# Performance work log

Hardware: AMD Instinct MI355X
Metric: run time of the kernel (lower is better)

## Reference

```python
import jax, jax.numpy as jnp
import numpy as np


def setup_inputs() -> dict:
    key = jax.random.key(0)
    k1, k2 = jax.random.split(key)
    n_nodes, d_feat, n_edges = 100000, 48, 1600000
    x = jax.random.normal(k1, (n_nodes, d_feat), dtype=jnp.float32)
    edge_index = jax.random.randint(k2, (2, n_edges), 0, n_nodes, dtype=jnp.int64)
    return {"x": x, "edge_index": edge_index, "batch_size": 65536}


def reference(x, edge_index, batch_size):
    # adj = SparseTensor.from_edge_index(edge_index): adj[row, col] = 1 with
    # row = edge_index[0] (src), col = edge_index[1] (dst).
    # adj.t() @ x  ->  out[i] = sum over edges (src -> i) of x[src]
    src, dst = edge_index[0], edge_index[1]
    n_nodes = x.shape[0]
    # memory-bound gather + scatter-add (SpMM, sum aggregation)
    x_neighbors_sum = jax.ops.segment_sum(x[src], dst, num_segments=n_nodes)
    node_labels = jnp.concatenate(
        (x[:batch_size, :], x_neighbors_sum[:batch_size, :]), axis=-1
    )
    return node_labels
```

## Files before the change

kernel.cpp:

```cpp
#include <hip/hip_runtime.h>
#include <hip/hip_fp16.h>

#define DFEAT 48
#define OUTW  96
#define NBINB 512
#define BINTH 512
#define EPT   7
#define SORTCAP 3584
#define NBUCK2 512
#define RBITS 7
#define NROWS 128
#define RAWCAP 2560
#define CSRCAP 2560


static __device__ __forceinline__ unsigned short f2h(float f) {
    __half h = __float2half_rn(f);
    return *reinterpret_cast<unsigned short*>(&h);
}

static __device__ __forceinline__ int wave_iscan(int v, int lane) {
    #pragma unroll
    for (int d = 1; d < 64; d <<= 1) {
        int tv = __shfl_up(v, d, 64);
        if (lane >= d) v += tv;
    }
    return v;
}

__global__ __launch_bounds__(BINTH)
void bin_k(const int* __restrict__ ei, int n_edges, int batch, int chunk,
           const float4* __restrict__ x4, int nx4, uint2* __restrict__ xh4,
           unsigned short* __restrict__ starts, unsigned int* __restrict__ regions,
           float4* __restrict__ out4, int use_half) {
    __shared__ int cnt[NBUCK2];
    __shared__ int cur[NBUCK2];
    __shared__ int wsum[BINTH / 64];
    __shared__ int totS;
    __shared__ unsigned int sorted[SORTCAP];
    const int t = threadIdx.x;
    const int b = blockIdx.x;
    const int lane = t & 63, wid = t >> 6;

    if (use_half) {
        const int batch12 = batch * 12;
        for (int i = b * BINTH + t; i < nx4; i += NBINB * BINTH) {
            float4 v = x4[i];
            xh4[i] = make_uint2((unsigned)f2h(v.x) | ((unsigned)f2h(v.y) << 16),
                                (unsigned)f2h(v.z) | ((unsigned)f2h(v.w) << 16));
            if (i < batch12) {
                int row = i / 12, cg = i - row * 12;
                out4[(size_t)row * 24 + cg] = v;
            }
        }
    }

    const int beg = b * chunk;
    const int end = min(beg + chunk, n_edges);

    unsigned int pay[EPT];
    int bkt[EPT];
    #pragma unroll
    for (int i = 0; i < EPT; i++) {
        bkt[i] = -1;
        int e = beg + t + i * BINTH;
        if (e < end) {
            int dst = ei[n_edges + e];
            if (dst < batch) {
                int src = ei[e];
                bkt[i] = dst >> RBITS;
                pay[i] = ((unsigned)(dst & (NROWS - 1)) << 17) | (unsigned)src;
            }
        }
    }
    cnt[t] = 0;
    __syncthreads();
    #pragma unroll
    for (int i = 0; i < EPT; i++)
        if (bkt[i] >= 0) atomicAdd(&cnt[bkt[i]], 1);
    __syncthreads();
    int v = cnt[t];
    int iv = wave_iscan(v, lane);
    if (lane == 63) wsum[wid] = iv;
    __syncthreads();
    if (t < BINTH / 64) {
        int wv = wsum[t];
        int sv = wave_iscan(wv, t);
        wsum[t] = sv - wv;
        if (t == BINTH / 64 - 1) totS = sv;
    }
    __syncthreads();
    int excl = iv - v + wsum[wid];
    int tot = totS;
    cur[t] = excl;
    starts[t * NBINB + b] = (unsigned short)excl;
    if (t == 0) starts[NBUCK2 * NBINB + b] = (unsigned short)tot;
    __syncthreads();
    #pragma unroll
    for (int i = 0; i < EPT; i++)
        if (bkt[i] >= 0) {
            int pos = atomicAdd(&cur[bkt[i]], 1);
            sorted[pos] = pay[i];
        }
    __syncthreads();
    unsigned int* reg = regions + (size_t)b * chunk;
    for (int i = t; i < tot; i += BINTH) reg[i] = sorted[i];
}

__global__ __launch_bounds__(1024)
void reduce_k(const float* __restrict__ x, const uint2* __restrict__ xh2,
              const unsigned short* __restrict__ starts,
              const unsigned int* __restrict__ regions,
              float* __restrict__ out, int batch, int chunk, int use_half) {
    __shared__ unsigned int raw[RAWCAP];
    __shared__ int csr[CSRCAP];
    __shared__ int cnt[NROWS], off[NROWS + 1], cur[NROWS];
    __shared__ int rbase[NBINB], rs[NBINB], rl[NBINB];
    __shared__ int wsum[16];
    __shared__ int totS;
    const int t = threadIdx.x;
    const int kb = blockIdx.x;
    const int lane = t & 63, wid = t >> 6;

    int s0 = 0, len = 0;
    if (t < NBINB) {
        s0 = starts[kb * NBINB + t];
        int s1 = starts[(kb + 1) * NBINB + t];
        len = s1 - s0;
    }
    int iv = wave_iscan(len, lane);
    if (lane == 63 && wid < 8) wsum[wid] = iv;
    __syncthreads();
    if (t < 8) {
        int wv = wsum[t];
        int sv = wave_iscan(wv, t);
        wsum[t] = sv - wv;
        if (t == 7) totS = sv;
    }
    __syncthreads();
    if (t < NBINB) {
        rbase[t] = iv - len + wsum[wid];
        rs[t] = s0;
        rl[t] = len;
    }
    __syncthreads();
    const int T = min(totS, RAWCAP);
    {
        int r = t >> 1, h = t & 1;
        int L = rl[r], base = rbase[r];
        const unsigned int* reg = regions + (size_t)r * chunk + rs[r];
        if (L <= 8) {
            #pragma unroll
            for (int i = 0; i < 4; i++) {
                int idx = h + 2 * i;
                if (idx < L) {
                    int p = base + idx;
                    if (p < RAWCAP) raw[p] = reg[idx];
                }
            }
        } else {
            for (int idx = h; idx < L; idx += 2) {
                int p = base + idx;
                if (p < RAWCAP) raw[p] = reg[idx];
            }
        }
    }
    if (t < NROWS) cnt[t] = 0;
    __syncthreads();
    for (int i = t; i < T; i += 1024) atomicAdd(&cnt[raw[i] >> 17], 1);
    __syncthreads();
    int v2 = (t < NROWS) ? cnt[t] : 0;
    int iv2 = wave_iscan(v2, lane);
    if (lane == 63 && wid < 2) wsum[wid] = iv2;
    __syncthreads();
    if (t == 0) {
        int a = wsum[0];
        off[NROWS] = a + wsum[1];
        wsum[1] = a;
        wsum[0] = 0;
    }
    __syncthreads();
    if (t < NROWS) {
        int excl = iv2 - v2 + wsum[wid];
        off[t] = excl;
        cur[t] = excl;
    }
    __syncthreads();
    for (int i = t; i < T; i += 1024) {
        unsigned int p = raw[i];
        int pos = atomicAdd(&cur[p >> 17], 1);
        if (pos < CSRCAP) csr[pos] = (int)(p & 0x1FFFFu) * 12;
    }
    __syncthreads();

    if (use_half) {
        const int g  = lane / 12;
        const int cg = lane - g * 12;
        const bool act = lane < 48;
        float4* out4 = (float4*)out;
        #pragma unroll
        for (int rr = 0; rr < 4; rr++) {
            const int ra = wid + 16 * rr;
            const int rb = ra + 64;
            const int rowA = kb * NROWS + ra;
            const int rowB = kb * NROWS + rb;
            const bool okA = rowA < batch, okB = rowB < batch;
            int e0a = 0, e1a = 0, e0b = 0, e1b = 0;
            if (okA) { e0a = off[ra]; e1a = min(off[ra + 1], CSRCAP); }
            if (okB) { e0b = off[rb]; e1b = min(off[rb + 1], CSRCAP); }
            float4 accA = make_float4(0.f, 0.f, 0.f, 0.f);
            float4 accB = make_float4(0.f, 0.f, 0.f, 0.f);
            int na = e1a - e0a, nb2 = e1b - e0b;
            int n = na > nb2 ? na : nb2;
            for (int k = 0; k < n; k += 8) {
                if (act) {
                    int a1 = e0a + k + g, a2 = e0a + k + 4 + g;
                    int b1 = e0b + k + g, b2 = e0b + k + 4 + g;
                    if (a1 < e1a) {
                        uint2 p = xh2[(size_t)csr[a1] + cg];
                        float2 f0 = __half22float2(*(const __half2*)&p.x);
                        float2 f1 = __half22float2(*(const __half2*)&p.y);
                        accA.x += f0.x; accA.y += f0.y; accA.z += f1.x; accA.w += f1.y;
                    }
                    if (b1 < e1b) {
                        uint2 p = xh2[(size_t)csr[b1] + cg];
                        float2 f0 = __half22float2(*(const __half2*)&p.x);
                        float2 f1 = __half22float2(*(const __half2*)&p.y);
                        accB.x += f0.x; accB.y += f0.y; accB.z += f1.x; accB.w += f1.y;
                    }
                    if (a2 < e1a) {
                        uint2 p = xh2[(size_t)csr[a2] + cg];
                        float2 f0 = __half22float2(*(const __half2*)&p.x);
                        float2 f1 = __half22float2(*(const __half2*)&p.y);
                        accA.x += f0.x; accA.y += f0.y; accA.z += f1.x; accA.w += f1.y;
                    }
                    if (b2 < e1b) {
                        uint2 p = xh2[(size_t)csr[b2] + cg];
                        float2 f0 = __half22float2(*(const __half2*)&p.x);
                        float2 f1 = __half22float2(*(const __half2*)&p.y);
                        accB.x += f0.x; accB.y += f0.y; accB.z += f1.x; accB.w += f1.y;
                    }
                }
            }
            float4 bb;
            bb.x = __shfl(accA.x, lane + 24); bb.y = __shfl(accA.y, lane + 24);
            bb.z = __shfl(accA.z, lane + 24); bb.w = __shfl(accA.w, lane + 24);
            if (lane < 24) { accA.x += bb.x; accA.y += bb.y; accA.z += bb.z; accA.w += bb.w; }
            bb.x = __shfl(accA.x, lane + 12); bb.y = __shfl(accA.y, lane + 12);
            bb.z = __shfl(accA.z, lane + 12); bb.w = __shfl(accA.w, lane + 12);
            if (lane < 12 && okA) {
                accA.x += bb.x; accA.y += bb.y; accA.z += bb.z; accA.w += bb.w;
                out4[(size_t)rowA * 24 + 12 + cg] = accA;
            }
            bb.x = __shfl(accB.x, lane + 24); bb.y = __shfl(accB.y, lane + 24);
            bb.z = __shfl(accB.z, lane + 24); bb.w = __shfl(accB.w, lane + 24);
            if (lane < 24) { accB.x += bb.x; accB.y += bb.y; accB.z += bb.z; accB.w += bb.w; }
            bb.x = __shfl(accB.x, lane + 12); bb.y = __shfl(accB.y, lane + 12);
            bb.z = __shfl(accB.z, lane + 12); bb.w = __shfl(accB.w, lane + 12);
            if (lane < 12 && okB) {
                accB.x += bb.x; accB.y += bb.y; accB.z += bb.z; accB.w += bb.w;
                out4[(size_t)rowB * 24 + 12 + cg] = accB;
            }
        }
    } else {
        if (lane < DFEAT) {
            for (int r = wid; r < NROWS; r += 16) {
                int row = kb * NROWS + r;
                if (row >= batch) break;
                int e0 = off[r], e1 = min(off[r + 1], CSRCAP);
                float acc = 0.f;
                for (int e = e0; e < e1; ++e)
                    acc += x[(size_t)csr[e] * 4 + lane];
                out[(size_t)row * OUTW + lane]         = x[(size_t)row * DFEAT + lane];
                out[(size_t)row * OUTW + DFEAT + lane] = acc;
            }
        }
    }
}


#define D4   12
#define ROW4 24

__global__ void init_out_kernel(const float4* __restrict__ x4,
                                float4* __restrict__ out4, int batch) {
    int idx = blockIdx.x * blockDim.x + threadIdx.x;
    int total = batch * ROW4;
    if (idx >= total) return;
    int row = idx / ROW4;
    int c   = idx - row * ROW4;
    float4 v;
    if (c < D4) v = x4[row * D4 + c];
    else        v = make_float4(0.f, 0.f, 0.f, 0.f);
    out4[idx] = v;
}

__global__ void scatter_edges_kernel(const float4* __restrict__ x4,
                                     const int* __restrict__ ei,
                                     float* __restrict__ out,
                                     int n_edges, int batch) {
    int tid = blockIdx.x * blockDim.x + threadIdx.x;
    int e = tid / D4;
    int q = tid - e * D4;
    if (e >= n_edges) return;
    int dst = ei[n_edges + e];
    if (dst >= batch) return;
    int src = ei[e];
    float4 v = x4[src * D4 + q];
    float* p = out + (size_t)dst * OUTW + DFEAT + q * 4;
    atomicAdd(p + 0, v.x);
    atomicAdd(p + 1, v.y);
    atomicAdd(p + 2, v.z);
    atomicAdd(p + 3, v.w);
}


extern "C" void kernel_launch(void* const* d_in, const int* in_sizes, int n_in,
                              void* d_out, int out_size, void* d_ws, size_t ws_size,
                              hipStream_t stream) {
    const float* x  = (const float*)d_in[0];
    const int*   ei = (const int*)d_in[1];
    float* out = (float*)d_out;

    const int n_edges = in_sizes[1] / 2;
    const int batch   = out_size / OUTW;
    const int n_nodes = in_sizes[0] / DFEAT;
    const int chunk   = (n_edges + NBINB - 1) / NBINB;
    const int nbuck   = (batch + NROWS - 1) / NROWS;
    const int nx4     = n_nodes * DFEAT / 4;

    size_t xh_bytes = ((size_t)n_nodes * DFEAT * sizeof(unsigned short) + 15) & ~(size_t)15;
    size_t starts_bytes = (size_t)(NBUCK2 + 1) * NBINB * sizeof(unsigned short);
    size_t reg_bytes = (size_t)NBINB * chunk * sizeof(unsigned int);
    size_t need_h = xh_bytes + starts_bytes + reg_bytes;
    size_t need_f = starts_bytes + reg_bytes;

    bool base_ok = chunk <= SORTCAP && chunk <= BINTH * EPT && chunk < 65536 &&
                   n_nodes <= (1 << 17) && batch <= NBUCK2 * NROWS &&
                   (n_nodes * DFEAT) % 4 == 0 && nbuck >= 1 && nbuck <= NBUCK2 &&
                   batch % NROWS == 0;

    if (base_ok && ws_size >= need_h) {
        unsigned short* xh = (unsigned short*)d_ws;
        unsigned short* starts = (unsigned short*)((char*)d_ws + xh_bytes);
        unsigned int* regions = (unsigned int*)((char*)d_ws + xh_bytes + starts_bytes);
        bin_k<<<NBINB, BINTH, 0, stream>>>(ei, n_edges, batch, chunk,
                                           (const float4*)x, nx4, (uint2*)xh,
                                           starts, regions, (float4*)out, 1);
        reduce_k<<<nbuck, 1024, 0, stream>>>(x, (const uint2*)xh, starts, regions,
                                             out, batch, chunk, 1);
    } else if (base_ok && ws_size >= need_f) {
        unsigned short* starts = (unsigned short*)d_ws;
        unsigned int* regions = (unsigned int*)((char*)d_ws + starts_bytes);
        bin_k<<<NBINB, BINTH, 0, stream>>>(ei, n_edges, batch, chunk,
                                           (const float4*)x, nx4, (uint2*)0,
                                           starts, regions, (float4*)out, 0);
        reduce_k<<<nbuck, 1024, 0, stream>>>(x, (const uint2*)0, starts, regions,
                                             out, batch, chunk, 0);
    } else {
        {
            int total = batch * ROW4;
            int grid = (total + 255) / 256;
            init_out_kernel<<<grid, 256, 0, stream>>>((const float4*)x,
                                                      (float4*)out, batch);
        }
        {
            long long total = (long long)n_edges * D4;
            long long grid = (total + 255) / 256;
            scatter_edges_kernel<<<(int)grid, 256, 0, stream>>>(
                (const float4*)x, ei, out, n_edges, batch);
        }
    }
}
```

Baseline: 119.6 us.

## Fuse bin and reduce kernels via cooperative launch with grid sync

Merges the binning and per-row reduction kernels into one cooperative kernel that separates the phases with a grid-wide barrier, falling back to two launches when cooperative launch is unavailable or occupancy is insufficient. The reduce phase is templated on thread count so it can run with 512 threads per block inside the fused kernel. The half-precision gather is also widened to 16-byte loads, with each edge split between A and B rows across half-waves. This removes one kernel launch and its boundary, at the cost of running the reduce phase with fewer threads per block and adding a grid barrier. The fp32 fallback's csr index scaling was also changed (stride 8 with a *6 row index), which looks inconsistent with that path.

```diff
diff --git a/kernel.cpp b/kernel.cpp
--- a/kernel.cpp
+++ b/kernel.cpp
@@ -1,5 +1,6 @@
 #include <hip/hip_runtime.h>
 #include <hip/hip_fp16.h>
+#include <hip/hip_cooperative_groups.h>
 
 #define DFEAT 48
 #define OUTW  96
@@ -28,18 +29,18 @@
     return v;
 }
 
-__global__ __launch_bounds__(BINTH)
-void bin_k(const int* __restrict__ ei, int n_edges, int batch, int chunk,
-           const float4* __restrict__ x4, int nx4, uint2* __restrict__ xh4,
-           unsigned short* __restrict__ starts, unsigned int* __restrict__ regions,
-           float4* __restrict__ out4, int use_half) {
+static __device__ __forceinline__ void bin_body(
+    const int* __restrict__ ei, int n_edges, int batch, int chunk,
+    const float4* __restrict__ x4, int nx4, uint2* __restrict__ xh4,
+    unsigned short* __restrict__ starts, unsigned int* __restrict__ regions,
+    float4* __restrict__ out4, int use_half, int b)
+{
     __shared__ int cnt[NBUCK2];
     __shared__ int cur[NBUCK2];
     __shared__ int wsum[BINTH / 64];
     __shared__ int totS;
     __shared__ unsigned int sorted[SORTCAP];
     const int t = threadIdx.x;
-    const int b = blockIdx.x;
     const int lane = t & 63, wid = t >> 6;
 
     if (use_half) {
@@ -107,11 +108,15 @@
     for (int i = t; i < tot; i += BINTH) reg[i] = sorted[i];
 }
 
-__global__ __launch_bounds__(1024)
-void reduce_k(const float* __restrict__ x, const uint2* __restrict__ xh2,
-              const unsigned short* __restrict__ starts,
-              const unsigned int* __restrict__ regions,
-              float* __restrict__ out, int batch, int chunk, int use_half) {
+template<int NT>
+static __device__ __forceinline__ void reduce_body(
+    const float* __restrict__ x, const uint4* __restrict__ xh4,
+    const unsigned short* __restrict__ starts,
+    const unsigned int* __restrict__ regions,
+    float* __restrict__ out, int batch, int chunk, int use_half, int kb)
+{
+    constexpr int NW  = NT / 64;
+    constexpr int TPR = NT / NBINB;
     __shared__ unsigned int raw[RAWCAP];
     __shared__ int csr[CSRCAP];
     __shared__ int cnt[NROWS], off[NROWS + 1], cur[NROWS];
@@ -119,7 +124,6 @@
     __shared__ int wsum[16];
     __shared__ int totS;
     const int t = threadIdx.x;
-    const int kb = blockIdx.x;
     const int lane = t & 63, wid = t >> 6;
 
     int s0 = 0, len = 0;
@@ -146,20 +150,11 @@
     __syncthreads();
     const int T = min(totS, RAWCAP);
     {
-        int r = t >> 1, h = t & 1;
-        int L = rl[r], base = rbase[r];
-        const unsigned int* reg = regions + (size_t)r * chunk + rs[r];
-        if (L <= 8) {
-            #pragma unroll
-            for (int i = 0; i < 4; i++) {
-                int idx = h + 2 * i;
-                if (idx < L) {
-                    int p = base + idx;
-                    if (p < RAWCAP) raw[p] = reg[idx];
-                }
-            }
-        } else {
-            for (int idx = h; idx < L; idx += 2) {
+        int r = t / TPR, h = t - r * TPR;
+        if (r < NBINB) {
+            int L = rl[r], base = rbase[r];
+            const unsigned int* reg = regions + (size_t)r * chunk + rs[r];
+            for (int idx = h; idx < L; idx += TPR) {
                 int p = base + idx;
                 if (p < RAWCAP) raw[p] = reg[idx];
             }
@@ -167,7 +162,7 @@
     }
     if (t < NROWS) cnt[t] = 0;
     __syncthreads();
-    for (int i = t; i < T; i += 1024) atomicAdd(&cnt[raw[i] >> 17], 1);
+    for (int i = t; i < T; i += NT) atomicAdd(&cnt[raw[i] >> 17], 1);
     __syncthreads();
     int v2 = (t < NROWS) ? cnt[t] : 0;
     int iv2 = wave_iscan(v2, lane);
@@ -186,21 +181,22 @@
         cur[t] = excl;
     }
     __syncthreads();
-    for (int i = t; i < T; i += 1024) {
+    for (int i = t; i < T; i += NT) {
         unsigned int p = raw[i];
         int pos = atomicAdd(&cur[p >> 17], 1);
-        if (pos < CSRCAP) csr[pos] = (int)(p & 0x1FFFFu) * 12;
+        if (pos < CSRCAP) csr[pos] = (int)(p & 0x1FFFFu) * 6;
     }
     __syncthreads();
 
     if (use_half) {
-        const int g  = lane / 12;
-        const int cg = lane - g * 12;
+        const int g   = lane / 6;
+        const int cg  = lane - g * 6;
         const bool act = lane < 48;
+        const bool isA = g < 4;
+        const int gg  = isA ? g : g - 4;
         float4* out4 = (float4*)out;
-        #pragma unroll
-        for (int rr = 0; rr < 4; rr++) {
-            const int ra = wid + 16 * rr;
+        for (int rr = 0; rr < 64 / NW; rr++) {
+            const int ra = wid + NW * rr;
             const int rb = ra + 64;
             const int rowA = kb * NROWS + ra;
             const int rowB = kb * NROWS + rb;
@@ -208,74 +204,99 @@
             int e0a = 0, e1a = 0, e0b = 0, e1b = 0;
             if (okA) { e0a = off[ra]; e1a = min(off[ra + 1], CSRCAP); }
             if (okB) { e0b = off[rb]; e1b = min(off[rb + 1], CSRCAP); }
-            float4 accA = make_float4(0.f, 0.f, 0.f, 0.f);
-            float4 accB = make_float4(0.f, 0.f, 0.f, 0.f);
-            int na = e1a - e0a, nb2 = e1b - e0b;
-            int n = na > nb2 ? na : nb2;
+            const int e0 = isA ? e0a : e0b;
+            const int e1 = isA ? e1a : e1b;
+            float a0=0.f,a1=0.f,a2=0.f,a3=0.f,a4=0.f,a5=0.f,a6=0.f,a7=0.f;
+            const int n = max(e1a - e0a, e1b - e0b);
             for (int k = 0; k < n; k += 8) {
-                if (act) {
-                    int a1 = e0a + k + g, a2 = e0a + k + 4 + g;
-                    int b1 = e0b + k + g, b2 = e0b + k + 4 + g;
-                    if (a1 < e1a) {
-                        uint2 p = xh2[(size_t)csr[a1] + cg];
-                        float2 f0 = __half22float2(*(const __half2*)&p.x);
-                        float2 f1 = __half22float2(*(const __half2*)&p.y);
-                        accA.x += f0.x; accA.y += f0.y; accA.z += f1.x; accA.w += f1.y;
-                    }
-                    if (b1 < e1b) {
-                        uint2 p = xh2[(size_t)csr[b1] + cg];
-                        float2 f0 = __half22float2(*(const __half2*)&p.x);
-                        float2 f1 = __half22float2(*(const __half2*)&p.y);
-                        accB.x += f0.x; accB.y += f0.y; accB.z += f1.x; accB.w += f1.y;
-                    }
-                    if (a2 < e1a) {
-                        uint2 p = xh2[(size_t)csr[a2] + cg];
-                        float2 f0 = __half22float2(*(const __half2*)&p.x);
-                        float2 f1 = __half22float2(*(const __half2*)&p.y);
-                        accA.x += f0.x; accA.y += f0.y; accA.z += f1.x; accA.w += f1.y;
-                    }
-                    if (b2 < e1b) {
-                        uint2 p = xh2[(size_t)csr[b2] + cg];
-                        float2 f0 = __half22float2(*(const __half2*)&p.x);
-                        float2 f1 = __half22float2(*(const __half2*)&p.y);
-                        accB.x += f0.x; accB.y += f0.y; accB.z += f1.x; accB.w += f1.y;
-                    }
+                int i1 = e0 + k + gg;
+                int i2 = i1 + 4;
+                if (act && i1 < e1) {
+                    uint4 p = xh4[(size_t)csr[i1] + cg];
+                    float2 f0 = __half22float2(*(const __half2*)&p.x);
+                    float2 f1 = __half22float2(*(const __half2*)&p.y);
+                    float2 f2 = __half22float2(*(const __half2*)&p.z);
+                    float2 f3 = __half22float2(*(const __half2*)&p.w);
+                    a0 += f0.x; a1 += f0.y; a2 += f1.x; a3 += f1.y;
+                    a4 += f2.x; a5 += f2.y; a6 += f3.x; a7 += f3.y;
                 }
-            }
-            float4 bb;
-            bb.x = __shfl(accA.x, lane + 24); bb.y = __shfl(accA.y, lane + 24);
-            bb.z = __shfl(accA.z, lane + 24); bb.w = __shfl(accA.w, lane + 24);
-            if (lane < 24) { accA.x += bb.x; accA.y += bb.y; accA.z += bb.z; accA.w += bb.w; }
-            bb.x = __shfl(accA.x, lane + 12); bb.y = __shfl(accA.y, lane + 12);
-            bb.z = __shfl(accA.z, lane + 12); bb.w = __shfl(accA.w, lane + 12);
-            if (lane < 12 && okA) {
-                accA.x += bb.x; accA.y += bb.y; accA.z += bb.z; accA.w += bb.w;
-                out4[(size_t)rowA * 24 + 12 + cg] = accA;
-            }
-            bb.x = __shfl(accB.x, lane + 24); bb.y = __shfl(accB.y, lane + 24);
-            bb.z = __shfl(accB.z, lane + 24); bb.w = __shfl(accB.w, lane + 24);
-            if (lane < 24) { accB.x += bb.x; accB.y += bb.y; accB.z += bb.z; accB.w += bb.w; }
-            bb.x = __shfl(accB.x, lane + 12); bb.y = __shfl(accB.y, lane + 12);
-            bb.z = __shfl(accB.z, lane + 12); bb.w = __shfl(accB.w, lane + 12);
-            if (lane < 12 && okB) {
-                accB.x += bb.x; accB.y += bb.y; accB.z += bb.z; accB.w += bb.w;
-                out4[(size_t)rowB * 24 + 12 + cg] = accB;
+                if (act && i2 < e1) {
+                    uint4 p = xh4[(size_t)csr[i2] + cg];
+                    float2 f0 = __half22float2(*(const __half2*)&p.x);
+                    float2 f1 = __half22float2(*(const __half2*)&p.y);
+                    float2 f2 = __half22float2(*(const __half2*)&p.z);
+                    float2 f3 = __half22float2(*(const __half2*)&p.w);
+                    a0 += f0.x; a1 += f0.y; a2 += f1.x; a3 += f1.y;
+                    a4 += f2.x; a5 += f2.y; a6 += f3.x; a7 += f3.y;
+                }
+            }
+            float b0,b1,b2,b3,b4,b5,b6,b7;
+            b0=__shfl(a0,lane+12); b1=__shfl(a1,lane+12);
+            b2=__shfl(a2,lane+12); b3=__shfl(a3,lane+12);
+            b4=__shfl(a4,lane+12); b5=__shfl(a5,lane+12);
+            b6=__shfl(a6,lane+12); b7=__shfl(a7,lane+12);
+            a0+=b0; a1+=b1; a2+=b2; a3+=b3; a4+=b4; a5+=b5; a6+=b6; a7+=b7;
+            b0=__shfl(a0,lane+6); b1=__shfl(a1,lane+6);
+            b2=__shfl(a2,lane+6); b3=__shfl(a3,lane+6);
+            b4=__shfl(a4,lane+6); b5=__shfl(a5,lane+6);
+            b6=__shfl(a6,lane+6); b7=__shfl(a7,lane+6);
+            a0+=b0; a1+=b1; a2+=b2; a3+=b3; a4+=b4; a5+=b5; a6+=b6; a7+=b7;
+            if (okA && lane < 6) {
+                out4[(size_t)rowA * 24 + 12 + cg * 2]     = make_float4(a0,a1,a2,a3);
+                out4[(size_t)rowA * 24 + 12 + cg * 2 + 1] = make_float4(a4,a5,a6,a7);
+            }
+            if (okB && lane >= 24 && lane < 30) {
+                out4[(size_t)rowB * 24 + 12 + cg * 2]     = make_float4(a0,a1,a2,a3);
+                out4[(size_t)rowB * 24 + 12 + cg * 2 + 1] = make_float4(a4,a5,a6,a7);
             }
         }
     } else {
         if (lane < DFEAT) {
-            for (int r = wid; r < NROWS; r += 16) {
+            for (int r = wid; r < NROWS; r += NW) {
                 int row = kb * NROWS + r;
                 if (row >= batch) break;
                 int e0 = off[r], e1 = min(off[r + 1], CSRCAP);
                 float acc = 0.f;
                 for (int e = e0; e < e1; ++e)
-                    acc += x[(size_t)csr[e] * 4 + lane];
+                    acc += x[(size_t)csr[e] * 8 + lane];
                 out[(size_t)row * OUTW + lane]         = x[(size_t)row * DFEAT + lane];
                 out[(size_t)row * OUTW + DFEAT + lane] = acc;
             }
         }
     }
+}
+
+
+__global__ __launch_bounds__(BINTH)
+void bin_k(const int* __restrict__ ei, int n_edges, int batch, int chunk,
+           const float4* __restrict__ x4, int nx4, uint2* __restrict__ xh4,
+           unsigned short* __restrict__ starts, unsigned int* __restrict__ regions,
+           float4* __restrict__ out4, int use_half) {
+    bin_body(ei, n_edges, batch, chunk, x4, nx4, xh4, starts, regions, out4,
+             use_half, blockIdx.x);
+}
+
+__global__ __launch_bounds__(1024)
+void reduce_k(const float* __restrict__ x, const uint4* __restrict__ xh4,
+              const unsigned short* __restrict__ starts,
+              const unsigned int* __restrict__ regions,
+              float* __restrict__ out, int batch, int chunk, int use_half) {
+    reduce_body<1024>(x, xh4, starts, regions, out, batch, chunk, use_half,
+                      blockIdx.x);
+}
+
+__global__ __launch_bounds__(BINTH, 4)
+void fused_k(const int* __restrict__ ei, int n_edges, int batch, int chunk,
+             const float4* __restrict__ x4, int nx4, unsigned short* xh,
+             unsigned short* starts, unsigned int* regions,
+             float* out, const float* __restrict__ x, int use_half) {
+    bin_body(ei, n_edges, batch, chunk, x4, nx4, (uint2*)xh, starts, regions,
+             (float4*)out, use_half, blockIdx.x);
+    cooperative_groups::this_grid().sync();
+    const int nbuck = (batch + NROWS - 1) / NROWS;
+    if ((int)blockIdx.x < nbuck)
+        reduce_body<BINTH>(x, (const uint4*)xh, starts, regions, out, batch,
+                           chunk, use_half, blockIdx.x);
 }
 
 
@@ -340,23 +361,73 @@
                    (n_nodes * DFEAT) % 4 == 0 && nbuck >= 1 && nbuck <= NBUCK2 &&
                    batch % NROWS == 0;
 
+    static int coop_state = -1;
+    if (coop_state < 0) {
+        int dev = 0;
+        hipGetDevice(&dev);
+        int cl = 0, ncu = 0, nb = 0;
+        hipDeviceGetAttribute(&cl, hipDeviceAttributeCooperativeLaunch, dev);
+        hipDeviceGetAttribute(&ncu, hipDeviceAttributeMultiprocessorCount, dev);
+        hipError_t oe = hipOccupancyMaxActiveBlocksPerMultiprocessor(
+            &nb, (const void*)fused_k, BINTH, 0);
+        coop_state = (cl && oe == hipSuccess && (long long)nb * ncu >= NBINB) ? 1 : 0;
+    }
+
     if (base_ok && ws_size >= need_h) {
         unsigned short* xh = (unsigned short*)d_ws;
         unsigned short* starts = (unsigned short*)((char*)d_ws + xh_bytes);
         unsigned int* regions = (unsigned int*)((char*)d_ws + xh_bytes + starts_bytes);
-        bin_k<<<NBINB, BINTH, 0, stream>>>(ei, n_edges, batch, chunk,
-                                           (const float4*)x, nx4, (uint2*)xh,
-                                           starts, regions, (float4*)out, 1);
-        reduce_k<<<nbuck, 1024, 0, stream>>>(x, (const uint2*)xh, starts, regions,
-                                             out, batch, chunk, 1);
+        bool done = false;
+        if (coop_state == 1) {
+            const int* ei_a = ei;
+            int ne_a = n_edges, ba_a = batch, ch_a = chunk, nx_a = nx4, uh_a = 1;
+            const float4* x4_a = (const float4*)x;
+            unsigned short* xh_a = xh;
+            unsigned short* st_a = starts;
+            unsigned int* rg_a = regions;
+            float* out_a = out;
+            const float* x_a = x;
+            void* args[12] = { &ei_a, &ne_a, &ba_a, &ch_a, &x4_a, &nx_a,
+                               &xh_a, &st_a, &rg_a, &out_a, &x_a, &uh_a };
+            hipError_t le = hipLaunchCooperativeKernel(
+                (const void*)fused_k, dim3(NBINB), dim3(BINTH), args, 0, stream);
+            done = (le == hipSuccess);
+            if (!done) coop_state = 0;
+        }
+        if (!done) {
+            bin_k<<<NBINB, BINTH, 0, stream>>>(ei, n_edges, batch, chunk,
+                                               (const float4*)x, nx4, (uint2*)xh,
+                                               starts, regions, (float4*)out, 1);
+            reduce_k<<<nbuck, 1024, 0, stream>>>(x, (const uint4*)xh, starts,
+                                                 regions, out, batch, chunk, 1);
+        }
     } else if (base_ok && ws_size >= need_f) {
         unsigned short* starts = (unsigned short*)d_ws;
         unsigned int* regions = (unsigned int*)((char*)d_ws + starts_bytes);
-        bin_k<<<NBINB, BINTH, 0, stream>>>(ei, n_edges, batch, chunk,
-                                           (const float4*)x, nx4, (uint2*)0,
-                                           starts, regions, (float4*)out, 0);
-        reduce_k<<<nbuck, 1024, 0, stream>>>(x, (const uint2*)0, starts, regions,
-                                             out, batch, chunk, 0);
+        bool done = false;
+        if (coop_state == 1) {
+            const int* ei_a = ei;
+            int ne_a = n_edges, ba_a = batch, ch_a = chunk, nx_a = nx4, uh_a = 0;
+            const float4* x4_a = (const float4*)x;
+            unsigned short* xh_a = nullptr;
+            unsigned short* st_a = starts;
+            unsigned int* rg_a = regions;
+            float* out_a = out;
+            const float* x_a = x;
+            void* args[12] = { &ei_a, &ne_a, &ba_a, &ch_a, &x4_a, &nx_a,
+                               &xh_a, &st_a, &rg_a, &out_a, &x_a, &uh_a };
+            hipError_t le = hipLaunchCooperativeKernel(
+                (const void*)fused_k, dim3(NBINB), dim3(BINTH), args, 0, stream);
+            done = (le == hipSuccess);
+            if (!done) coop_state = 0;
+        }
+        if (!done) {
+            bin_k<<<NBINB, BINTH, 0, stream>>>(ei, n_edges, batch, chunk,
+                                               (const float4*)x, nx4, (uint2*)0,
+                                               starts, regions, (float4*)out, 0);
+            reduce_k<<<nbuck, 1024, 0, stream>>>(x, (const uint4*)0, starts,
+                                                 regions, out, batch, chunk, 0);
+        }
     } else {
         {
             int total = batch * ROW4;
```

Result: slower. 213.9 us (+78.9%).

## Widen half-precision gathers to 16-byte loads and add nontemporal loads/stores

Applied to the files above, without the earlier changes.

The reduce kernel now gathers each fp16 neighbor row with 6 lanes using 16-byte uint4 loads instead of 12 lanes with 8-byte loads. Each wave processes two output rows split across lane groups, which makes the cross-lane reduction shorter. Streaming reads of edge indices, x, and the region buffers, along with output stores, now use nontemporal builtins so they do not pollute cache. The fp32 fallback path index scaling was changed to *8, which looks wrong (x is indexed as csr*8 where csr = src*6 gives 48*src) but it does not run with the default workspace.

```diff
diff --git a/kernel.cpp b/kernel.cpp
--- a/kernel.cpp
+++ b/kernel.cpp
@@ -13,6 +13,8 @@
 #define RAWCAP 2560
 #define CSRCAP 2560
 
+
+typedef float        f4v __attribute__((ext_vector_type(4)));
 
 static __device__ __forceinline__ unsigned short f2h(float f) {
     __half h = __float2half_rn(f);
@@ -45,12 +47,12 @@
     if (use_half) {
         const int batch12 = batch * 12;
         for (int i = b * BINTH + t; i < nx4; i += NBINB * BINTH) {
-            float4 v = x4[i];
+            f4v v = __builtin_nontemporal_load((const f4v*)(x4 + i));
             xh4[i] = make_uint2((unsigned)f2h(v.x) | ((unsigned)f2h(v.y) << 16),
                                 (unsigned)f2h(v.z) | ((unsigned)f2h(v.w) << 16));
             if (i < batch12) {
                 int row = i / 12, cg = i - row * 12;
-                out4[(size_t)row * 24 + cg] = v;
+                __builtin_nontemporal_store(v, (f4v*)(out4 + (size_t)row * 24 + cg));
             }
         }
     }
@@ -65,9 +67,9 @@
         bkt[i] = -1;
         int e = beg + t + i * BINTH;
         if (e < end) {
-            int dst = ei[n_edges + e];
+            int dst = __builtin_nontemporal_load(ei + n_edges + e);
             if (dst < batch) {
-                int src = ei[e];
+                int src = __builtin_nontemporal_load(ei + e);
                 bkt[i] = dst >> RBITS;
                 pay[i] = ((unsigned)(dst & (NROWS - 1)) << 17) | (unsigned)src;
             }
@@ -108,7 +110,7 @@
 }
 
 __global__ __launch_bounds__(1024)
-void reduce_k(const float* __restrict__ x, const uint2* __restrict__ xh2,
+void reduce_k(const float* __restrict__ x, const uint4* __restrict__ xh4,
               const unsigned short* __restrict__ starts,
               const unsigned int* __restrict__ regions,
               float* __restrict__ out, int batch, int chunk, int use_half) {
@@ -155,13 +157,13 @@
                 int idx = h + 2 * i;
                 if (idx < L) {
                     int p = base + idx;
-                    if (p < RAWCAP) raw[p] = reg[idx];
+                    if (p < RAWCAP) raw[p] = __builtin_nontemporal_load(reg + idx);
                 }
             }
         } else {
             for (int idx = h; idx < L; idx += 2) {
                 int p = base + idx;
-                if (p < RAWCAP) raw[p] = reg[idx];
+                if (p < RAWCAP) raw[p] = __builtin_nontemporal_load(reg + idx);
             }
         }
     }
@@ -189,14 +191,16 @@
     for (int i = t; i < T; i += 1024) {
         unsigned int p = raw[i];
         int pos = atomicAdd(&cur[p >> 17], 1);
-        if (pos < CSRCAP) csr[pos] = (int)(p & 0x1FFFFu) * 12;
+        if (pos < CSRCAP) csr[pos] = (int)(p & 0x1FFFFu) * 6;
     }
     __syncthreads();
 
     if (use_half) {
-        const int g  = lane / 12;
-        const int cg = lane - g * 12;
+        const int g   = lane / 6;
+        const int cg  = lane - g * 6;
         const bool act = lane < 48;
+        const bool isA = g < 4;
+        const int gg  = isA ? g : g - 4;
         float4* out4 = (float4*)out;
         #pragma unroll
         for (int rr = 0; rr < 4; rr++) {
@@ -208,58 +212,54 @@
             int e0a = 0, e1a = 0, e0b = 0, e1b = 0;
             if (okA) { e0a = off[ra]; e1a = min(off[ra + 1], CSRCAP); }
             if (okB) { e0b = off[rb]; e1b = min(off[rb + 1], CSRCAP); }
-            float4 accA = make_float4(0.f, 0.f, 0.f, 0.f);
-            float4 accB = make_float4(0.f, 0.f, 0.f, 0.f);
-            int na = e1a - e0a, nb2 = e1b - e0b;
-            int n = na > nb2 ? na : nb2;
+            const int e0 = isA ? e0a : e0b;
+            const int e1 = isA ? e1a : e1b;
+            float a0=0.f,a1=0.f,a2=0.f,a3=0.f,a4=0.f,a5=0.f,a6=0.f,a7=0.f;
+            const int n = max(e1a - e0a, e1b - e0b);
             for (int k = 0; k < n; k += 8) {
-                if (act) {
-                    int a1 = e0a + k + g, a2 = e0a + k + 4 + g;
-                    int b1 = e0b + k + g, b2 = e0b + k + 4 + g;
-                    if (a1 < e1a) {
-                        uint2 p = xh2[(size_t)csr[a1] + cg];
-                        float2 f0 = __half22float2(*(const __half2*)&p.x);
-                        float2 f1 = __half22float2(*(const __half2*)&p.y);
-                        accA.x += f0.x; accA.y += f0.y; accA.z += f1.x; accA.w += f1.y;
-                    }
-                    if (b1 < e1b) {
-                        uint2 p = xh2[(size_t)csr[b1] + cg];
-                        float2 f0 = __half22float2(*(const __half2*)&p.x);
-                        float2 f1 = __half22float2(*(const __half2*)&p.y);
-                        accB.x += f0.x; accB.y += f0.y; accB.z += f1.x; accB.w += f1.y;
-                    }
-                    if (a2 < e1a) {
-                        uint2 p = xh2[(size_t)csr[a2] + cg];
-                        float2 f0 = __half22float2(*(const __half2*)&p.x);
-                        float2 f1 = __half22float2(*(const __half2*)&p.y);
-                        accA.x += f0.x; accA.y += f0.y; accA.z += f1.x; accA.w += f1.y;
-                    }
-                    if (b2 < e1b) {
-                        uint2 p = xh2[(size_t)csr[b2] + cg];
-                        float2 f0 = __half22float2(*(const __half2*)&p.x);
-                        float2 f1 = __half22float2(*(const __half2*)&p.y);
-                        accB.x += f0.x; accB.y += f0.y; accB.z += f1.x; accB.w += f1.y;
-                    }
+                int i1 = e0 + k + gg;
+                int i2 = i1 + 4;
+                if (act && i1 < e1) {
+                    uint4 p = xh4[(size_t)csr[i1] + cg];
+                    float2 f0 = __half22float2(*(const __half2*)&p.x);
+                    float2 f1 = __half22float2(*(const __half2*)&p.y);
+                    float2 f2 = __half22float2(*(const __half2*)&p.z);
+                    float2 f3 = __half22float2(*(const __half2*)&p.w);
+                    a0 += f0.x; a1 += f0.y; a2 += f1.x; a3 += f1.y;
+                    a4 += f2.x; a5 += f2.y; a6 += f3.x; a7 += f3.y;
                 }
-            }
-            float4 bb;
-            bb.x = __shfl(accA.x, lane + 24); bb.y = __shfl(accA.y, lane + 24);
-            bb.z = __shfl(accA.z, lane + 24); bb.w = __shfl(accA.w, lane + 24);
-            if (lane < 24) { accA.x += bb.x; accA.y += bb.y; accA.z += bb.z; accA.w += bb.w; }
-            bb.x = __shfl(accA.x, lane + 12); bb.y = __shfl(accA.y, lane + 12);
-            bb.z = __shfl(accA.z, lane + 12); bb.w = __shfl(accA.w, lane + 12);
-            if (lane < 12 && okA) {
-                accA.x += bb.x; accA.y += bb.y; accA.z += bb.z; accA.w += bb.w;
-                out4[(size_t)rowA * 24 + 12 + cg] = accA;
-            }
-            bb.x = __shfl(accB.x, lane + 24); bb.y = __shfl(accB.y, lane + 24);
-            bb.z = __shfl(accB.z, lane + 24); bb.w = __shfl(accB.w, lane + 24);
-            if (lane < 24) { accB.x += bb.x; accB.y += bb.y; accB.z += bb.z; accB.w += bb.w; }
-            bb.x = __shfl(accB.x, lane + 12); bb.y = __shfl(accB.y, lane + 12);
-            bb.z = __shfl(accB.z, lane + 12); bb.w = __shfl(accB.w, lane + 12);
-            if (lane < 12 && okB) {
-                accB.x += bb.x; accB.y += bb.y; accB.z += bb.z; accB.w += bb.w;
-                out4[(size_t)rowB * 24 + 12 + cg] = accB;
+                if (act && i2 < e1) {
+                    uint4 p = xh4[(size_t)csr[i2] + cg];
+                    float2 f0 = __half22float2(*(const __half2*)&p.x);
+                    float2 f1 = __half22float2(*(const __half2*)&p.y);
+                    float2 f2 = __half22float2(*(const __half2*)&p.z);
+                    float2 f3 = __half22float2(*(const __half2*)&p.w);
+                    a0 += f0.x; a1 += f0.y; a2 += f1.x; a3 += f1.y;
+                    a4 += f2.x; a5 += f2.y; a6 += f3.x; a7 += f3.y;
+                }
+            }
+            float b0,b1,b2,b3,b4,b5,b6,b7;
+            b0=__shfl(a0,lane+12); b1=__shfl(a1,lane+12);
+            b2=__shfl(a2,lane+12); b3=__shfl(a3,lane+12);
+            b4=__shfl(a4,lane+12); b5=__shfl(a5,lane+12);
+            b6=__shfl(a6,lane+12); b7=__shfl(a7,lane+12);
+            a0+=b0; a1+=b1; a2+=b2; a3+=b3; a4+=b4; a5+=b5; a6+=b6; a7+=b7;
+            b0=__shfl(a0,lane+6); b1=__shfl(a1,lane+6);
+            b2=__shfl(a2,lane+6); b3=__shfl(a3,lane+6);
+            b4=__shfl(a4,lane+6); b5=__shfl(a5,lane+6);
+            b6=__shfl(a6,lane+6); b7=__shfl(a7,lane+6);
+            a0+=b0; a1+=b1; a2+=b2; a3+=b3; a4+=b4; a5+=b5; a6+=b6; a7+=b7;
+            if (okA && lane < 6) {
+                f4v w0 = {a0, a1, a2, a3};
+                f4v w1 = {a4, a5, a6, a7};
+                __builtin_nontemporal_store(w0, (f4v*)(out4 + (size_t)rowA * 24 + 12 + cg * 2));
+                __builtin_nontemporal_store(w1, (f4v*)(out4 + (size_t)rowA * 24 + 12 + cg * 2 + 1));
+            }
+            if (okB && lane >= 24 && lane < 30) {
+                f4v w0 = {a0, a1, a2, a3};
+                f4v w1 = {a4, a5, a6, a7};
+                __builtin_nontemporal_store(w0, (f4v*)(out4 + (size_t)rowB * 24 + 12 + cg * 2));
+                __builtin_nontemporal_store(w1, (f4v*)(out4 + (size_t)rowB * 24 + 12 + cg * 2 + 1));
             }
         }
     } else {
@@ -270,7 +270,7 @@
                 int e0 = off[r], e1 = min(off[r + 1], CSRCAP);
                 float acc = 0.f;
                 for (int e = e0; e < e1; ++e)
-                    acc += x[(size_t)csr[e] * 4 + lane];
+                    acc += x[(size_t)csr[e] * 8 + lane];
                 out[(size_t)row * OUTW + lane]         = x[(size_t)row * DFEAT + lane];
                 out[(size_t)row * OUTW + DFEAT + lane] = acc;
             }
@@ -347,7 +347,7 @@
         bin_k<<<NBINB, BINTH, 0, stream>>>(ei, n_edges, batch, chunk,
                                            (const float4*)x, nx4, (uint2*)xh,
                                            starts, regions, (float4*)out, 1);
-        reduce_k<<<nbuck, 1024, 0, stream>>>(x, (const uint2*)xh, starts, regions,
+        reduce_k<<<nbuck, 1024, 0, stream>>>(x, (const uint4*)xh, starts, regions,
                                              out, batch, chunk, 1);
     } else if (base_ok && ws_size >= need_f) {
         unsigned short* starts = (unsigned short*)d_ws;
@@ -355,7 +355,7 @@
         bin_k<<<NBINB, BINTH, 0, stream>>>(ei, n_edges, batch, chunk,
                                            (const float4*)x, nx4, (uint2*)0,
                                            starts, regions, (float4*)out, 0);
-        reduce_k<<<nbuck, 1024, 0, stream>>>(x, (const uint2*)0, starts, regions,
+        reduce_k<<<nbuck, 1024, 0, stream>>>(x, (const uint4*)0, starts, regions,
                                              out, batch, chunk, 0);
     } else {
         {
```

Result: slower. 124.5 us (+4.1%).
